# Kernel tuning notes

Hardware: AMD Instinct MI355X
Metric: run time of the kernel (lower is better)

Reference implementation:

```python
import jax, jax.numpy as jnp
import numpy as np

B, TV, TE = 128, 32, 64
VOCAB, EMB, H, REPR, NET, MAXLEN = 1024, 256, 512, 128, 8, 32


def setup_inputs() -> dict:
    key = jax.random.key(0)
    ks = jax.random.split(key, 26)
    g = lambda i, shape: jax.random.normal(ks[i], shape, dtype=jnp.float32) * 0.05
    return dict(
        input_vertex=jax.random.randint(ks[0], (B, TV), 0, VOCAB),
        input_edge=jax.random.randint(ks[1], (B, TE, 3), 0, NET),
        vertex_emb=g(2, (VOCAB, EMB)),
        v_Wi=g(3, (3 * H, EMB)), v_Wh=g(4, (3 * H, H)), v_bi=g(5, (3 * H,)), v_bh=g(6, (3 * H,)),
        vout_W=g(7, (VOCAB, H)), vout_b=g(8, (VOCAB,)),
        vrep_W=g(9, (REPR, H)), vrep_b=g(10, (REPR,)),
        edge_emb=g(11, (MAXLEN, EMB)),
        e_Wi=g(12, (3 * H, 2 * EMB)), e_Wh=g(13, (3 * H, H)), e_bi=g(14, (3 * H,)), e_bh=g(15, (3 * H,)),
        erep_W=g(16, (REPR, H)), erep_b=g(17, (REPR,)),
        etype_W=g(18, (NET, REPR)), etype_b=g(19, (NET,)),
        src_w=g(20, (REPR,)), src_b=g(21, ()),
        dst_w=g(22, (REPR,)), dst_b=g(23, ()),
    )


def _gru_scan(X, Wi, Wh, bi, bh):
    # X: [T, B, D] -> hidden states [T, B, H]; torch GRUCell gate order r,z,n
    gi = jnp.einsum('tbd,gd->tbg', X, Wi) + bi  # precompute input projections
    h0 = jnp.zeros((X.shape[1], Wh.shape[1]), X.dtype)

    def step(h, gi_t):
        gh = h @ Wh.T + bh
        ir, iz, inn = jnp.split(gi_t, 3, axis=-1)
        hr, hz, hn = jnp.split(gh, 3, axis=-1)
        r = jax.nn.sigmoid(ir + hr)
        z = jax.nn.sigmoid(iz + hz)
        n = jnp.tanh(inn + r * hn)
        h_new = (1.0 - z) * n + z * h
        return h_new, h_new

    _, hs = jax.lax.scan(step, h0, gi)
    return hs


def reference(input_vertex, input_edge, vertex_emb, v_Wi, v_Wh, v_bi, v_bh,
              vout_W, vout_b, vrep_W, vrep_b, edge_emb, e_Wi, e_Wh, e_bi, e_bh,
              erep_W, erep_b, etype_W, etype_b, src_w, src_b, dst_w, dst_b):
    # ---- vertex RNN ----
    Ve = vertex_emb[input_vertex].transpose(1, 0, 2)          # [Tv, B, emb]
    hv = _gru_scan(Ve, v_Wi, v_Wh, v_bi, v_bh)                # [Tv, B, H]
    O_vertex = jnp.einsum('tbh,vh->bvt', hv, vout_W) + vout_b[None, :, None]  # [B, vocab, Tv]
    vrep = jnp.einsum('tbh,rh->tbr', hv, vrep_W) + vrep_b     # [Tv, B, repr]

    # ---- edge RNN ----
    E = jnp.concatenate([edge_emb[input_edge[:, :, 0]],
                         edge_emb[input_edge[:, :, 1]]], axis=2)  # [B, Te, 2*emb]
    he = _gru_scan(E.transpose(1, 0, 2), e_Wi, e_Wh, e_bi, e_bh)  # [Te, B, H]
    e = jnp.einsum('tbh,rh->tbr', he, erep_W) + erep_b            # [Te, B, repr]
    O_edge_type = jnp.einsum('ebr,kr->bke', e, etype_W) + etype_b[None, :, None]  # [B, n_et, Te]

    # ---- edge-vertex additive attention: tanh(e + v) ----
    u = jnp.tanh(e[:, None] + vrep[None])                     # [Te, Tv, B, repr]
    osrc = jnp.einsum('evbr,r->bve', u, src_w) + src_b        # [B, Tv, Te]
    odst = jnp.einsum('evbr,r->bve', u, dst_w) + dst_b        # [B, Tv, Te]
    O_edge = jnp.stack([osrc, odst], axis=2)                  # [B, Tv, 2, Te]

    return O_vertex, O_edge, O_edge_type
```

## Files before the change

kernel.cpp:

```cpp
#include <hip/hip_runtime.h>
#include <hip/hip_bf16.h>


typedef __bf16 bf16_t;
typedef bf16_t bf16x8 __attribute__((ext_vector_type(8)));
typedef bf16_t bf16x4 __attribute__((ext_vector_type(4)));
typedef float  f32x4  __attribute__((ext_vector_type(4)));

#define OFF_GIV  0ull
#define OFF_GIE  6291456ull
#define OFF_HV   18874368ull
#define OFF_HE   20971520ull
#define OFF_VREP 25165824ull
#define OFF_EREP 25690112ull
#define OFF_HBUF 26738688ull
#define FLAG_BYTE_OFF 54001664ull
#define GICNT_BYTE_OFF 54001920ull
#define OFF_CVT  27002880ull
#define CVT_VEMB  0ull
#define CVT_EEMB  262144ull
#define CVT_VWI   270336ull
#define CVT_EWI   663552ull
#define CVT_VWH   1449984ull
#define CVT_EWH   2236416ull
#define CVT_VOUT  3022848ull
#define CVT_VREPW 3547136ull
#define CVT_EREPW 3612672ull

#define OUT_OV 0ull
#define OUT_OE 4194304ull
#define OUT_OT 4718592ull

__device__ __forceinline__ float fsigmoid(float x) {
    float e = __builtin_amdgcn_exp2f(-x * 1.4426950408889634f);
    return __builtin_amdgcn_rcpf(1.0f + e);
}
__device__ __forceinline__ float ftanh(float x) {
    x = fminf(x, 15.0f);
    float e = __builtin_amdgcn_exp2f(x * 2.8853900817779268f);
    return (e - 1.0f) * __builtin_amdgcn_rcpf(e + 1.0f);
}

__global__ __launch_bounds__(256) void prep_kernel(
    const float* __restrict__ vemb, const float* __restrict__ eemb,
    const float* __restrict__ vwi,  const float* __restrict__ ewi,
    const float* __restrict__ vwh,  const float* __restrict__ ewh,
    const float* __restrict__ voutw, const float* __restrict__ vrepw,
    const float* __restrict__ erepw, bf16_t* __restrict__ cvt,
    int* __restrict__ gicnt)
{
    int blk = blockIdx.x;
    if (blk >= 3592) {
        if (threadIdx.x < 128) gicnt[threadIdx.x] = 0;
        return;
    }
    const float* src; bf16_t* dst; int lb;
    if (blk < 256)       { src = vemb;  dst = cvt + CVT_VEMB;  lb = blk; }
    else if (blk < 264)  { src = eemb;  dst = cvt + CVT_EEMB;  lb = blk - 256; }
    else if (blk < 648)  { src = vwi;   dst = cvt + CVT_VWI;   lb = blk - 264; }
    else if (blk < 1416) { src = ewi;   dst = cvt + CVT_EWI;   lb = blk - 648; }
    else if (blk < 2184) { src = vwh;   dst = cvt + CVT_VWH;   lb = blk - 1416; }
    else if (blk < 2952) { src = ewh;   dst = cvt + CVT_EWH;   lb = blk - 2184; }
    else if (blk < 3464) { src = voutw; dst = cvt + CVT_VOUT;  lb = blk - 2952; }
    else if (blk < 3528) { src = vrepw; dst = cvt + CVT_VREPW; lb = blk - 3464; }
    else                 { src = erepw; dst = cvt + CVT_EREPW; lb = blk - 3528; }
    int idx = lb * 1024 + threadIdx.x * 4;
    float4 v = *(const float4*)(src + idx);
    bf16x4 o;
    o[0] = (bf16_t)v.x; o[1] = (bf16_t)v.y; o[2] = (bf16_t)v.z; o[3] = (bf16_t)v.w;
    *(bf16x4*)(dst + idx) = o;
}

template<int GATHER, int K>
__device__ __forceinline__ void produce_gi(
    const bf16_t* __restrict__ W, const float* __restrict__ bias,
    bf16_t* __restrict__ C, const int* __restrict__ gidx,
    const bf16_t* __restrict__ emb, int* __restrict__ cnt, int bx, int nbase)
{
    constexpr int K32 = K / 32;
    const int tid = threadIdx.x, lane = tid & 63, wv = tid >> 6;
    const int r16 = lane & 15, quad = lane >> 4, koff = quad * 8;
    const int mbase = bx * 512 + wv * 64;

    const bf16_t* ap0[4];
    const bf16_t* ap1[4];
#pragma unroll
    for (int i = 0; i < 4; ++i) {
        int row = mbase + i * 16 + r16;
        int b = row & 127, t = row >> 7;
        if (GATHER == 1) {
            ap0[i] = emb + (size_t)gidx[b * 32 + t] * 256 + koff;
            ap1[i] = ap0[i];
        } else {
            int c = (b * 64 + t) * 3;
            ap0[i] = emb + (size_t)gidx[c] * 256 + koff;
            ap1[i] = emb + (size_t)gidx[c + 1] * 256 + koff;
        }
    }
    const bf16_t* bp[4];
#pragma unroll
    for (int j = 0; j < 4; ++j)
        bp[j] = W + (size_t)(nbase + j * 16 + r16) * K + koff;

    f32x4 acc[4][4];
#pragma unroll
    for (int i = 0; i < 4; ++i)
#pragma unroll
        for (int j = 0; j < 4; ++j) acc[i][j] = (f32x4){0.f, 0.f, 0.f, 0.f};

    for (int kc = 0; kc < K32; ++kc) {
        bf16x8 a[4], b[4];
#pragma unroll
        for (int i = 0; i < 4; ++i) {
            const bf16_t* p;
            if (GATHER == 2) p = (kc < 8) ? (ap0[i] + kc * 32) : (ap1[i] + (kc - 8) * 32);
            else             p = ap0[i] + kc * 32;
            a[i] = *(const bf16x8*)p;
        }
#pragma unroll
        for (int j = 0; j < 4; ++j) b[j] = *(const bf16x8*)(bp[j] + kc * 32);
#pragma unroll
        for (int i = 0; i < 4; ++i)
#pragma unroll
            for (int j = 0; j < 4; ++j)
                acc[i][j] = __builtin_amdgcn_mfma_f32_16x16x32_bf16(a[i], b[j], acc[i][j], 0, 0, 0);
    }

#pragma unroll
    for (int j = 0; j < 4; ++j) {
        int col = nbase + j * 16 + r16;
        float bf = bias[col];
#pragma unroll
        for (int i = 0; i < 4; ++i) {
#pragma unroll
            for (int q = 0; q < 4; ++q) {
                int row = mbase + i * 16 + quad * 4 + q;
                bf16_t hb = (bf16_t)(acc[i][j][q] + bf);
                __hip_atomic_store((unsigned short*)(C + (size_t)row * 1536 + col),
                                   __builtin_bit_cast(unsigned short, hb),
                                   __ATOMIC_RELAXED, __HIP_MEMORY_SCOPE_AGENT);
            }
        }
    }
    __builtin_amdgcn_s_waitcnt(0);
    __syncthreads();
    if (tid < 4)
        __hip_atomic_fetch_add(&cnt[bx * 4 + tid], 1,
                               __ATOMIC_RELAXED, __HIP_MEMORY_SCOPE_AGENT);
}

template<int OUTMODE, int K>
__device__ __forceinline__ void consume_gemm(
    const bf16_t* __restrict__ A, const bf16_t* __restrict__ W,
    const float* __restrict__ bias, void* __restrict__ Cv,
    int N, int bx, int nbase)
{
    constexpr int K32 = K / 32;
    const int tid = threadIdx.x, lane = tid & 63, wv = tid >> 6;
    const int r16 = lane & 15, quad = lane >> 4, koff = quad * 8;
    const int mbase = bx * 512 + wv * 64;

    const bf16_t* ap[4];
#pragma unroll
    for (int i = 0; i < 4; ++i)
        ap[i] = A + (size_t)(mbase + i * 16 + r16) * K + koff;
    const bf16_t* bp[4];
#pragma unroll
    for (int j = 0; j < 4; ++j)
        bp[j] = W + (size_t)(nbase + j * 16 + r16) * K + koff;

    f32x4 acc[4][4];
#pragma unroll
    for (int i = 0; i < 4; ++i)
#pragma unroll
        for (int j = 0; j < 4; ++j) acc[i][j] = (f32x4){0.f, 0.f, 0.f, 0.f};

    for (int kc = 0; kc < K32; ++kc) {
        bf16x8 a[4], b[4];
#pragma unroll
        for (int i = 0; i < 4; ++i) a[i] = *(const bf16x8*)(ap[i] + kc * 32);
#pragma unroll
        for (int j = 0; j < 4; ++j) b[j] = *(const bf16x8*)(bp[j] + kc * 32);
#pragma unroll
        for (int i = 0; i < 4; ++i)
#pragma unroll
            for (int j = 0; j < 4; ++j)
                acc[i][j] = __builtin_amdgcn_mfma_f32_16x16x32_bf16(a[i], b[j], acc[i][j], 0, 0, 0);
    }

#pragma unroll
    for (int j = 0; j < 4; ++j) {
        int col = nbase + j * 16 + r16;
        float bf = bias[col];
#pragma unroll
        for (int i = 0; i < 4; ++i) {
            int rowq = mbase + i * 16 + quad * 4;
            if (OUTMODE == 1) {
                int b = rowq >> 5, t0 = rowq & 31;
                float4 v4;
                v4.x = acc[i][j][0] + bf; v4.y = acc[i][j][1] + bf;
                v4.z = acc[i][j][2] + bf; v4.w = acc[i][j][3] + bf;
                *(float4*)((float*)Cv + ((size_t)(b * 1024) + col) * 32 + t0) = v4;
            } else {
                bf16_t* C = (bf16_t*)Cv;
#pragma unroll
                for (int q = 0; q < 4; ++q)
                    C[(size_t)(rowq + q) * N + col] = (bf16_t)(acc[i][j][q] + bf);
            }
        }
    }
}

__device__ __forceinline__ void gate_on(int* p, int thresh) {
    if (threadIdx.x == 0) {
        while (__hip_atomic_load(p, __ATOMIC_RELAXED,
                                 __HIP_MEMORY_SCOPE_AGENT) < thresh)
            __builtin_amdgcn_s_sleep(8);
    }
    __syncthreads();
    asm volatile("" ::: "memory");
}

__global__ __launch_bounds__(512) void fused_scan(
    bf16_t* __restrict__ giV, bf16_t* __restrict__ giE,
    const bf16_t* __restrict__ WhV, const bf16_t* __restrict__ WhE,
    const float* __restrict__ bhV, const float* __restrict__ bhE,
    bf16_t* __restrict__ hV, bf16_t* __restrict__ hE,
    bf16_t* __restrict__ hbuf, int* __restrict__ flags, int* __restrict__ gicnt,
    const int* __restrict__ ivtx, const int* __restrict__ iedg,
    const bf16_t* __restrict__ vemb, const bf16_t* __restrict__ eemb,
    const bf16_t* __restrict__ vwi, const bf16_t* __restrict__ ewi,
    const float* __restrict__ vbi, const float* __restrict__ ebi,
    const bf16_t* __restrict__ voutw, const float* __restrict__ voutb,
    const bf16_t* __restrict__ vrepw, const float* __restrict__ vrepb,
    const bf16_t* __restrict__ erepw, const float* __restrict__ erepb,
    bf16_t* __restrict__ vrep, bf16_t* __restrict__ erep,
    float* __restrict__ out)
{
    __shared__ __align__(16) bf16_t hbf[2][16][520];
    __shared__ char ldspad[31744];
    const int bid = blockIdx.x;
    if ((int)gridDim.x < 0) ldspad[threadIdx.x] = 0;

    if (bid >= 64) {
        if (bid < 256) {
            int g2 = bid - 64;
            produce_gi<1, 256>(vwi, vbi, giV, ivtx, vemb, gicnt, g2 & 7, (g2 >> 3) * 64);
        } else if (bid < 640) {
            int g3 = bid - 256;
            produce_gi<2, 512>(ewi, ebi, giE, iedg, eemb, gicnt + 32, g3 & 15, (g3 >> 4) * 64);
        } else if (bid < 784) {
            gate_on(&gicnt[96], 32);
            if (bid < 768) {
                int cb = bid - 640;
                consume_gemm<1, 512>(hV, voutw, voutb, out, 1024, cb & 7, (cb >> 3) * 64);
            } else {
                int cb = bid - 768;
                consume_gemm<0, 512>(hV, vrepw, vrepb, vrep, 128, cb & 7, (cb >> 3) * 64);
            }
        } else {
            gate_on(&gicnt[97], 32);
            int cb = bid - 784;
            consume_gemm<0, 512>(hE, erepw, erepb, erep, 128, cb & 15, (cb >> 4) * 64);
        }
        return;
    }

    const int role = bid >> 5;
    const int lb   = bid & 31;
    const int g    = lb & 7;
    const int s    = lb >> 3;
    const bf16_t* gi = role ? giE : giV;
    const bf16_t* Wh = role ? WhE : WhV;
    const float*  bh = role ? bhE : bhV;
    bf16_t* hout = role ? hE : hV;
    const int T = role ? 64 : 32;
    const int slot = role * 8 + g;
    bf16_t* buf0 = hbuf + (size_t)slot * 2 * 8192;
    int* fl = flags + slot * 4;
    int* gc = role ? (gicnt + 32) : gicnt;
    int* done = role ? &gicnt[97] : &gicnt[96];
    const int bb = g * 16;

    const int tid = threadIdx.x, lane = tid & 63, wv = tid >> 6;
    const int r16 = lane & 15, quad = lane >> 4, koff = quad * 8;
    const int j = s * 128 + wv * 16 + r16;
    const int rs0 = (s + 1) & 3, rs1 = (s + 2) & 3, rs2 = (s + 3) & 3;

    bf16x8 wfrag[3][16];
#pragma unroll
    for (int gate = 0; gate < 3; ++gate) {
        const bf16_t* wrow = Wh + ((size_t)(gate * 512 + j)) * 512 + koff;
#pragma unroll
        for (int kc = 0; kc < 16; ++kc)
            wfrag[gate][kc] = *(const bf16x8*)(wrow + kc * 32);
    }
    const float bhr = bh[j], bhz = bh[512 + j], bhn = bh[1024 + j];
    float hq[4] = {0.f, 0.f, 0.f, 0.f};

    for (int i = tid; i < 16 * 512; i += 512)
        hbf[0][i >> 9][i & 511] = (bf16_t)0.f;

    const int arow = tid >> 5, au = tid & 31;

    for (int t = 0; t < T; ++t) {
        if (wv == 0) {
            while (__hip_atomic_load(&gc[t], __ATOMIC_RELAXED,
                                     __HIP_MEMORY_SCOPE_AGENT) < 24)
                __builtin_amdgcn_s_sleep(2);
        }
        __syncthreads();
        asm volatile("" ::: "memory");

        float gv[3][4];
#pragma unroll
        for (int gg = 0; gg < 3; ++gg)
#pragma unroll
            for (int q = 0; q < 4; ++q)
                gv[gg][q] = (float)gi[((size_t)(t * 128 + bb + quad * 4 + q)) * 1536
                                      + gg * 512 + j];

        if (t > 0) {
            if (wv == 1) {
                while (!__all((int)(__hip_atomic_load(&fl[lane & 3], __ATOMIC_RELAXED,
                                                      __HIP_MEMORY_SCOPE_AGENT) >= t))) { }
            }
            __syncthreads();
            asm volatile("" ::: "memory");
            unsigned long long* src = (unsigned long long*)(buf0 + (size_t)(t & 1) * 8192);
            unsigned long long vv[3];
            vv[0] = __hip_atomic_load(src + arow * 128 + rs0 * 32 + au, __ATOMIC_RELAXED, __HIP_MEMORY_SCOPE_AGENT);
            vv[1] = __hip_atomic_load(src + arow * 128 + rs1 * 32 + au, __ATOMIC_RELAXED, __HIP_MEMORY_SCOPE_AGENT);
            vv[2] = __hip_atomic_load(src + arow * 128 + rs2 * 32 + au, __ATOMIC_RELAXED, __HIP_MEMORY_SCOPE_AGENT);
            *(unsigned long long*)&hbf[t & 1][arow][rs0 * 128 + au * 4] = vv[0];
            *(unsigned long long*)&hbf[t & 1][arow][rs1 * 128 + au * 4] = vv[1];
            *(unsigned long long*)&hbf[t & 1][arow][rs2 * 128 + au * 4] = vv[2];
        }
        __syncthreads();

        const bf16_t (*cur)[520] = hbf[t & 1];
        f32x4 ar = {0.f,0.f,0.f,0.f}, az = {0.f,0.f,0.f,0.f}, an = {0.f,0.f,0.f,0.f};
#pragma unroll
        for (int kc = 0; kc < 16; ++kc) {
            bf16x8 a = *(const bf16x8*)&cur[r16][kc * 32 + koff];
            ar = __builtin_amdgcn_mfma_f32_16x16x32_bf16(a, wfrag[0][kc], ar, 0, 0, 0);
            az = __builtin_amdgcn_mfma_f32_16x16x32_bf16(a, wfrag[1][kc], az, 0, 0, 0);
            an = __builtin_amdgcn_mfma_f32_16x16x32_bf16(a, wfrag[2][kc], an, 0, 0, 0);
        }

        bf16_t hb4[4];
#pragma unroll
        for (int q = 0; q < 4; ++q) {
            float r = fsigmoid(gv[0][q] + ar[q] + bhr);
            float z = fsigmoid(gv[1][q] + az[q] + bhz);
            float n = ftanh(gv[2][q] + r * (an[q] + bhn));
            float hnew = (1.0f - z) * n + z * hq[q];
            hq[q] = hnew;
            hb4[q] = (bf16_t)hnew;
        }

        bf16_t (*nxt)[520] = hbf[(t + 1) & 1];
#pragma unroll
        for (int q = 0; q < 4; ++q) nxt[quad * 4 + q][j] = hb4[q];

        if (t + 1 < T) {
            bf16_t* dstg = buf0 + (size_t)((t + 1) & 1) * 8192;
#pragma unroll
            for (int q = 0; q < 4; ++q)
                __hip_atomic_store((unsigned short*)(dstg + (quad * 4 + q) * 512 + j),
                                   __builtin_bit_cast(unsigned short, hb4[q]),
                                   __ATOMIC_RELAXED, __HIP_MEMORY_SCOPE_AGENT);
            __builtin_amdgcn_s_waitcnt(0);
            __syncthreads();
            if (tid == 0)
                __hip_atomic_store(&fl[s], t + 1,
                                   __ATOMIC_RELAXED, __HIP_MEMORY_SCOPE_AGENT);
        } else {
            __syncthreads();
        }
#pragma unroll
        for (int q = 0; q < 4; ++q)
            __hip_atomic_store(
                (unsigned short*)(hout + ((size_t)((bb + quad * 4 + q) * T + t)) * 512 + j),
                __builtin_bit_cast(unsigned short, hb4[q]),
                __ATOMIC_RELAXED, __HIP_MEMORY_SCOPE_AGENT);
    }

    __builtin_amdgcn_s_waitcnt(0);
    __syncthreads();
    if (tid == 0)
        __hip_atomic_fetch_add(done, 1, __ATOMIC_RELAXED, __HIP_MEMORY_SCOPE_AGENT);
}

__global__ __launch_bounds__(256) void etype_kernel(
    const bf16_t* __restrict__ erep, const float* __restrict__ W,
    const float* __restrict__ bias, float* __restrict__ out)
{
    int o = blockIdx.x * 256 + threadIdx.x;
    int te = o & 63, k = (o >> 6) & 7, b = o >> 9;
    float sacc = bias[k];
    const bf16_t* e = erep + ((size_t)(b * 64 + te)) * 128;
    const float* w = W + k * 128;
#pragma unroll 8
    for (int r = 0; r < 128; ++r) sacc += (float)e[r] * w[r];
    out[OUT_OT + o] = sacc;
}

__global__ __launch_bounds__(256) void attn_kernel(
    const bf16_t* __restrict__ erep, const bf16_t* __restrict__ vrep,
    const float* __restrict__ src_w, const float* __restrict__ src_b,
    const float* __restrict__ dst_w, const float* __restrict__ dst_b,
    float* __restrict__ out)
{
    int b = blockIdx.x >> 1, half = blockIdx.x & 1;
    __shared__ float es[32][129], vs[32][129], swf[128], dwf[128];
    int tid = threadIdx.x;
    for (int f = tid; f < 32 * 128; f += 256) {
        int i = f >> 7, r = f & 127;
        es[i][r] = (float)erep[((size_t)(b * 64 + half * 32 + i)) * 128 + r];
        vs[i][r] = (float)vrep[((size_t)(b * 32 + i)) * 128 + r];
    }
    if (tid < 128) { swf[tid] = src_w[tid]; dwf[tid] = dst_w[tid]; }
    __syncthreads();
    float sb = src_b[0], db = dst_b[0];
    for (int p = tid; p < 1024; p += 256) {
        int te = p & 31, tv = p >> 5;
        float sacc = 0.f, dacc = 0.f;
#pragma unroll 4
        for (int r = 0; r < 128; ++r) {
            float u = ftanh(es[te][r] + vs[tv][r]);
            sacc += u * swf[r];
            dacc += u * dwf[r];
        }
        int teg = half * 32 + te;
        size_t base = OUT_OE + ((size_t)(b * 32 + tv) * 2) * 64;
        out[base + teg]      = sacc + sb;
        out[base + 64 + teg] = dacc + db;
    }
}

extern "C" void kernel_launch(void* const* d_in, const int* in_sizes, int n_in,
                              void* d_out, int out_size, void* d_ws, size_t ws_size,
                              hipStream_t stream)
{
    const int*   input_vertex = (const int*)d_in[0];
    const int*   input_edge   = (const int*)d_in[1];
    const float* vertex_emb   = (const float*)d_in[2];
    const float* v_Wi  = (const float*)d_in[3];
    const float* v_Wh  = (const float*)d_in[4];
    const float* v_bi  = (const float*)d_in[5];
    const float* v_bh  = (const float*)d_in[6];
    const float* vout_W = (const float*)d_in[7];
    const float* vout_b = (const float*)d_in[8];
    const float* vrep_W = (const float*)d_in[9];
    const float* vrep_b = (const float*)d_in[10];
    const float* edge_emb = (const float*)d_in[11];
    const float* e_Wi  = (const float*)d_in[12];
    const float* e_Wh  = (const float*)d_in[13];
    const float* e_bi  = (const float*)d_in[14];
    const float* e_bh  = (const float*)d_in[15];
    const float* erep_W = (const float*)d_in[16];
    const float* erep_b = (const float*)d_in[17];
    const float* etype_W = (const float*)d_in[18];
    const float* etype_b = (const float*)d_in[19];
    const float* src_w = (const float*)d_in[20];
    const float* src_b = (const float*)d_in[21];
    const float* dst_w = (const float*)d_in[22];
    const float* dst_b = (const float*)d_in[23];

    bf16_t* ws   = (bf16_t*)d_ws;
    bf16_t* giV  = ws + OFF_GIV;
    bf16_t* giE  = ws + OFF_GIE;
    bf16_t* hV   = ws + OFF_HV;
    bf16_t* hE   = ws + OFF_HE;
    bf16_t* vrep = ws + OFF_VREP;
    bf16_t* erep = ws + OFF_EREP;
    bf16_t* hbuf = ws + OFF_HBUF;
    bf16_t* cvt  = ws + OFF_CVT;
    int*    flags = (int*)((char*)d_ws + FLAG_BYTE_OFF);
    int*    gicnt = (int*)((char*)d_ws + GICNT_BYTE_OFF);
    float*  out  = (float*)d_out;

    prep_kernel<<<3593, 256, 0, stream>>>(vertex_emb, edge_emb, v_Wi, e_Wi, v_Wh, e_Wh,
                                          vout_W, vrep_W, erep_W, cvt, gicnt);

    fused_scan<<<816, 512, 0, stream>>>(
        giV, giE, cvt + CVT_VWH, cvt + CVT_EWH, v_bh, e_bh, hV, hE,
        hbuf, flags, gicnt, input_vertex, input_edge,
        cvt + CVT_VEMB, cvt + CVT_EEMB, cvt + CVT_VWI, cvt + CVT_EWI,
        v_bi, e_bi,
        cvt + CVT_VOUT, vout_b, cvt + CVT_VREPW, vrep_b,
        cvt + CVT_EREPW, erep_b, vrep, erep, out);

    etype_kernel<<<256, 256, 0, stream>>>(erep, etype_W, etype_b, out);
    attn_kernel<<<256, 256, 0, stream>>>(erep, vrep, src_w, src_b, dst_w, dst_b, out);
}
```

Before: 447.7 us.

## Split fused persistent scan into separate produce, GRU scan and consume kernels

Replaces the single persistent fused kernel, which overlapped input-projection GEMMs, the recurrent scans and the output GEMMs through atomic counters, with three separate launches. The GRU scan now spreads each batch group over 8 blocks instead of 4, and each block splits the K dimension between two wave halves that are reduced through shared memory. This halves the per-wave recurrent weight registers and gives more parallelism per step, at the cost of an extra LDS reduction and barrier each step, more cross-block flag polling, and losing the overlap between the producer GEMM and the scan.

```diff
diff --git a/kernel.cpp b/kernel.cpp
--- a/kernel.cpp
+++ b/kernel.cpp
@@ -15,7 +15,6 @@
 #define OFF_EREP 25690112ull
 #define OFF_HBUF 26738688ull
 #define FLAG_BYTE_OFF 54001664ull
-#define GICNT_BYTE_OFF 54001920ull
 #define OFF_CVT  27002880ull
 #define CVT_VEMB  0ull
 #define CVT_EEMB  262144ull
@@ -46,14 +45,9 @@
     const float* __restrict__ vwi,  const float* __restrict__ ewi,
     const float* __restrict__ vwh,  const float* __restrict__ ewh,
     const float* __restrict__ voutw, const float* __restrict__ vrepw,
-    const float* __restrict__ erepw, bf16_t* __restrict__ cvt,
-    int* __restrict__ gicnt)
+    const float* __restrict__ erepw, bf16_t* __restrict__ cvt)
 {
     int blk = blockIdx.x;
-    if (blk >= 3592) {
-        if (threadIdx.x < 128) gicnt[threadIdx.x] = 0;
-        return;
-    }
     const float* src; bf16_t* dst; int lb;
     if (blk < 256)       { src = vemb;  dst = cvt + CVT_VEMB;  lb = blk; }
     else if (blk < 264)  { src = eemb;  dst = cvt + CVT_EEMB;  lb = blk - 256; }
@@ -75,7 +69,7 @@
 __device__ __forceinline__ void produce_gi(
     const bf16_t* __restrict__ W, const float* __restrict__ bias,
     bf16_t* __restrict__ C, const int* __restrict__ gidx,
-    const bf16_t* __restrict__ emb, int* __restrict__ cnt, int bx, int nbase)
+    const bf16_t* __restrict__ emb, int bx, int nbase)
 {
     constexpr int K32 = K / 32;
     const int tid = threadIdx.x, lane = tid & 63, wv = tid >> 6;
@@ -135,18 +129,160 @@
 #pragma unroll
             for (int q = 0; q < 4; ++q) {
                 int row = mbase + i * 16 + quad * 4 + q;
-                bf16_t hb = (bf16_t)(acc[i][j][q] + bf);
-                __hip_atomic_store((unsigned short*)(C + (size_t)row * 1536 + col),
-                                   __builtin_bit_cast(unsigned short, hb),
+                C[(size_t)row * 1536 + col] = (bf16_t)(acc[i][j][q] + bf);
+            }
+        }
+    }
+}
+
+__global__ __launch_bounds__(512) void produce_kernel(
+    bf16_t* __restrict__ giV, bf16_t* __restrict__ giE,
+    const int* __restrict__ ivtx, const int* __restrict__ iedg,
+    const bf16_t* __restrict__ vemb, const bf16_t* __restrict__ eemb,
+    const bf16_t* __restrict__ vwi, const bf16_t* __restrict__ ewi,
+    const float* __restrict__ vbi, const float* __restrict__ ebi)
+{
+    int bid = blockIdx.x;
+    if (bid < 192) {
+        produce_gi<1, 256>(vwi, vbi, giV, ivtx, vemb, bid & 7, (bid >> 3) * 64);
+    } else {
+        int g3 = bid - 192;
+        produce_gi<2, 512>(ewi, ebi, giE, iedg, eemb, g3 & 15, (g3 >> 4) * 64);
+    }
+}
+
+__global__ __launch_bounds__(512)
+__attribute__((amdgpu_waves_per_eu(2, 2)))
+void gru_scan(
+    const bf16_t* __restrict__ giV, const bf16_t* __restrict__ giE,
+    const bf16_t* __restrict__ WhV, const bf16_t* __restrict__ WhE,
+    const float* __restrict__ bhV, const float* __restrict__ bhE,
+    bf16_t* __restrict__ hV, bf16_t* __restrict__ hE,
+    bf16_t* __restrict__ hbuf, int* __restrict__ flags)
+{
+    __shared__ __align__(16) bf16_t hbf[2][16][520];
+    __shared__ __align__(16) f32x4 red[4][3][64];
+    const int bid = blockIdx.x;
+
+    const int role = bid >> 6;
+    const int lb   = bid & 63;
+    const int g    = lb & 7;
+    const int s    = lb >> 3;
+    const bf16_t* gi = role ? giE : giV;
+    const bf16_t* Wh = role ? WhE : WhV;
+    const float*  bh = role ? bhE : bhV;
+    bf16_t* hout = role ? hE : hV;
+    const int T = role ? 64 : 32;
+    const int slot = role * 8 + g;
+    bf16_t* buf0 = hbuf + (size_t)slot * 2 * 8192;
+    int* fl = flags + slot * 8;
+    const int bb = g * 16;
+
+    const int tid = threadIdx.x, lane = tid & 63, wv = tid >> 6;
+    const int team = wv >> 1, half = wv & 1;
+    const int r16 = lane & 15, quad = lane >> 4, koff = quad * 8;
+    const int j = s * 64 + team * 16 + r16;
+    const int kbase = half * 256;
+
+    bf16x8 wfrag[3][8];
+#pragma unroll
+    for (int gate = 0; gate < 3; ++gate) {
+        const bf16_t* wrow = Wh + ((size_t)(gate * 512 + j)) * 512 + kbase + koff;
+#pragma unroll
+        for (int kc = 0; kc < 8; ++kc)
+            wfrag[gate][kc] = *(const bf16x8*)(wrow + kc * 32);
+    }
+    const float bhr = bh[j], bhz = bh[512 + j], bhn = bh[1024 + j];
+    float hq[4] = {0.f, 0.f, 0.f, 0.f};
+
+    for (int i = tid; i < 16 * 512; i += 512)
+        hbf[0][i >> 9][i & 511] = (bf16_t)0.f;
+
+    for (int t = 0; t < T; ++t) {
+        if (t > 0) {
+            if (wv == 1) {
+                while (!__all((int)(__hip_atomic_load(&fl[lane & 7], __ATOMIC_RELAXED,
+                                                      __HIP_MEMORY_SCOPE_AGENT) >= t))) { }
+            }
+            __syncthreads();
+            asm volatile("" ::: "memory");
+            unsigned long long* src = (unsigned long long*)(buf0 + (size_t)(t & 1) * 8192);
+#pragma unroll
+            for (int k = 0; k < 4; ++k) {
+                int u = tid + k * 512;
+                unsigned long long vv = __hip_atomic_load(src + u, __ATOMIC_RELAXED,
+                                                          __HIP_MEMORY_SCOPE_AGENT);
+                *(unsigned long long*)&hbf[t & 1][u >> 7][(u & 127) * 4] = vv;
+            }
+        }
+        __syncthreads();
+
+        float gv[3][4];
+        if (half == 0) {
+#pragma unroll
+            for (int gg = 0; gg < 3; ++gg)
+#pragma unroll
+                for (int q = 0; q < 4; ++q)
+                    gv[gg][q] = (float)gi[((size_t)(t * 128 + bb + quad * 4 + q)) * 1536
+                                          + gg * 512 + j];
+        }
+
+        const bf16_t (*cur)[520] = hbf[t & 1];
+        f32x4 ar = {0.f,0.f,0.f,0.f}, az = {0.f,0.f,0.f,0.f}, an = {0.f,0.f,0.f,0.f};
+#pragma unroll
+        for (int kc = 0; kc < 8; ++kc) {
+            bf16x8 a = *(const bf16x8*)&cur[r16][kbase + kc * 32 + koff];
+            ar = __builtin_amdgcn_mfma_f32_16x16x32_bf16(a, wfrag[0][kc], ar, 0, 0, 0);
+            az = __builtin_amdgcn_mfma_f32_16x16x32_bf16(a, wfrag[1][kc], az, 0, 0, 0);
+            an = __builtin_amdgcn_mfma_f32_16x16x32_bf16(a, wfrag[2][kc], an, 0, 0, 0);
+        }
+
+        if (half == 1) {
+            red[team][0][lane] = ar;
+            red[team][1][lane] = az;
+            red[team][2][lane] = an;
+        }
+        __syncthreads();
+
+        bf16_t hb4[4];
+        if (half == 0) {
+            ar += red[team][0][lane];
+            az += red[team][1][lane];
+            an += red[team][2][lane];
+#pragma unroll
+            for (int q = 0; q < 4; ++q) {
+                float r = fsigmoid(gv[0][q] + ar[q] + bhr);
+                float z = fsigmoid(gv[1][q] + az[q] + bhz);
+                float n = ftanh(gv[2][q] + r * (an[q] + bhn));
+                float hnew = (1.0f - z) * n + z * hq[q];
+                hq[q] = hnew;
+                hb4[q] = (bf16_t)hnew;
+            }
+            if (t + 1 < T) {
+                bf16_t* dstg = buf0 + (size_t)((t + 1) & 1) * 8192;
+#pragma unroll
+                for (int q = 0; q < 4; ++q)
+                    __hip_atomic_store((unsigned short*)(dstg + (quad * 4 + q) * 512 + j),
+                                       __builtin_bit_cast(unsigned short, hb4[q]),
+                                       __ATOMIC_RELAXED, __HIP_MEMORY_SCOPE_AGENT);
+            }
+        }
+
+        if (t + 1 < T) {
+            __builtin_amdgcn_s_waitcnt(0);
+            __syncthreads();
+            if (tid == 0)
+                __hip_atomic_store(&fl[s], t + 1,
                                    __ATOMIC_RELAXED, __HIP_MEMORY_SCOPE_AGENT);
-            }
-        }
-    }
-    __builtin_amdgcn_s_waitcnt(0);
-    __syncthreads();
-    if (tid < 4)
-        __hip_atomic_fetch_add(&cnt[bx * 4 + tid], 1,
-                               __ATOMIC_RELAXED, __HIP_MEMORY_SCOPE_AGENT);
+        } else {
+            __syncthreads();
+        }
+        if (half == 0) {
+#pragma unroll
+            for (int q = 0; q < 4; ++q)
+                hout[((size_t)((bb + quad * 4 + q) * T + t)) * 512 + j] = hb4[q];
+        }
+    }
 }
 
 template<int OUTMODE, int K>
@@ -211,185 +347,24 @@
     }
 }
 
-__device__ __forceinline__ void gate_on(int* p, int thresh) {
-    if (threadIdx.x == 0) {
-        while (__hip_atomic_load(p, __ATOMIC_RELAXED,
-                                 __HIP_MEMORY_SCOPE_AGENT) < thresh)
-            __builtin_amdgcn_s_sleep(8);
-    }
-    __syncthreads();
-    asm volatile("" ::: "memory");
-}
-
-__global__ __launch_bounds__(512) void fused_scan(
-    bf16_t* __restrict__ giV, bf16_t* __restrict__ giE,
-    const bf16_t* __restrict__ WhV, const bf16_t* __restrict__ WhE,
-    const float* __restrict__ bhV, const float* __restrict__ bhE,
-    bf16_t* __restrict__ hV, bf16_t* __restrict__ hE,
-    bf16_t* __restrict__ hbuf, int* __restrict__ flags, int* __restrict__ gicnt,
-    const int* __restrict__ ivtx, const int* __restrict__ iedg,
-    const bf16_t* __restrict__ vemb, const bf16_t* __restrict__ eemb,
-    const bf16_t* __restrict__ vwi, const bf16_t* __restrict__ ewi,
-    const float* __restrict__ vbi, const float* __restrict__ ebi,
+__global__ __launch_bounds__(512) void consume_kernel(
+    const bf16_t* __restrict__ hV, const bf16_t* __restrict__ hE,
     const bf16_t* __restrict__ voutw, const float* __restrict__ voutb,
     const bf16_t* __restrict__ vrepw, const float* __restrict__ vrepb,
     const bf16_t* __restrict__ erepw, const float* __restrict__ erepb,
     bf16_t* __restrict__ vrep, bf16_t* __restrict__ erep,
     float* __restrict__ out)
 {
-    __shared__ __align__(16) bf16_t hbf[2][16][520];
-    __shared__ char ldspad[31744];
-    const int bid = blockIdx.x;
-    if ((int)gridDim.x < 0) ldspad[threadIdx.x] = 0;
-
-    if (bid >= 64) {
-        if (bid < 256) {
-            int g2 = bid - 64;
-            produce_gi<1, 256>(vwi, vbi, giV, ivtx, vemb, gicnt, g2 & 7, (g2 >> 3) * 64);
-        } else if (bid < 640) {
-            int g3 = bid - 256;
-            produce_gi<2, 512>(ewi, ebi, giE, iedg, eemb, gicnt + 32, g3 & 15, (g3 >> 4) * 64);
-        } else if (bid < 784) {
-            gate_on(&gicnt[96], 32);
-            if (bid < 768) {
-                int cb = bid - 640;
-                consume_gemm<1, 512>(hV, voutw, voutb, out, 1024, cb & 7, (cb >> 3) * 64);
-            } else {
-                int cb = bid - 768;
-                consume_gemm<0, 512>(hV, vrepw, vrepb, vrep, 128, cb & 7, (cb >> 3) * 64);
-            }
-        } else {
-            gate_on(&gicnt[97], 32);
-            int cb = bid - 784;
-            consume_gemm<0, 512>(hE, erepw, erepb, erep, 128, cb & 15, (cb >> 4) * 64);
-        }
-        return;
-    }
-
-    const int role = bid >> 5;
-    const int lb   = bid & 31;
-    const int g    = lb & 7;
-    const int s    = lb >> 3;
-    const bf16_t* gi = role ? giE : giV;
-    const bf16_t* Wh = role ? WhE : WhV;
-    const float*  bh = role ? bhE : bhV;
-    bf16_t* hout = role ? hE : hV;
-    const int T = role ? 64 : 32;
-    const int slot = role * 8 + g;
-    bf16_t* buf0 = hbuf + (size_t)slot * 2 * 8192;
-    int* fl = flags + slot * 4;
-    int* gc = role ? (gicnt + 32) : gicnt;
-    int* done = role ? &gicnt[97] : &gicnt[96];
-    const int bb = g * 16;
-
-    const int tid = threadIdx.x, lane = tid & 63, wv = tid >> 6;
-    const int r16 = lane & 15, quad = lane >> 4, koff = quad * 8;
-    const int j = s * 128 + wv * 16 + r16;
-    const int rs0 = (s + 1) & 3, rs1 = (s + 2) & 3, rs2 = (s + 3) & 3;
-
-    bf16x8 wfrag[3][16];
-#pragma unroll
-    for (int gate = 0; gate < 3; ++gate) {
-        const bf16_t* wrow = Wh + ((size_t)(gate * 512 + j)) * 512 + koff;
-#pragma unroll
-        for (int kc = 0; kc < 16; ++kc)
-            wfrag[gate][kc] = *(const bf16x8*)(wrow + kc * 32);
-    }
-    const float bhr = bh[j], bhz = bh[512 + j], bhn = bh[1024 + j];
-    float hq[4] = {0.f, 0.f, 0.f, 0.f};
-
-    for (int i = tid; i < 16 * 512; i += 512)
-        hbf[0][i >> 9][i & 511] = (bf16_t)0.f;
-
-    const int arow = tid >> 5, au = tid & 31;
-
-    for (int t = 0; t < T; ++t) {
-        if (wv == 0) {
-            while (__hip_atomic_load(&gc[t], __ATOMIC_RELAXED,
-                                     __HIP_MEMORY_SCOPE_AGENT) < 24)
-                __builtin_amdgcn_s_sleep(2);
-        }
-        __syncthreads();
-        asm volatile("" ::: "memory");
-
-        float gv[3][4];
-#pragma unroll
-        for (int gg = 0; gg < 3; ++gg)
-#pragma unroll
-            for (int q = 0; q < 4; ++q)
-                gv[gg][q] = (float)gi[((size_t)(t * 128 + bb + quad * 4 + q)) * 1536
-                                      + gg * 512 + j];
-
-        if (t > 0) {
-            if (wv == 1) {
-                while (!__all((int)(__hip_atomic_load(&fl[lane & 3], __ATOMIC_RELAXED,
-                                                      __HIP_MEMORY_SCOPE_AGENT) >= t))) { }
-            }
-            __syncthreads();
-            asm volatile("" ::: "memory");
-            unsigned long long* src = (unsigned long long*)(buf0 + (size_t)(t & 1) * 8192);
-            unsigned long long vv[3];
-            vv[0] = __hip_atomic_load(src + arow * 128 + rs0 * 32 + au, __ATOMIC_RELAXED, __HIP_MEMORY_SCOPE_AGENT);
-            vv[1] = __hip_atomic_load(src + arow * 128 + rs1 * 32 + au, __ATOMIC_RELAXED, __HIP_MEMORY_SCOPE_AGENT);
-            vv[2] = __hip_atomic_load(src + arow * 128 + rs2 * 32 + au, __ATOMIC_RELAXED, __HIP_MEMORY_SCOPE_AGENT);
-            *(unsigned long long*)&hbf[t & 1][arow][rs0 * 128 + au * 4] = vv[0];
-            *(unsigned long long*)&hbf[t & 1][arow][rs1 * 128 + au * 4] = vv[1];
-            *(unsigned long long*)&hbf[t & 1][arow][rs2 * 128 + au * 4] = vv[2];
-        }
-        __syncthreads();
-
-        const bf16_t (*cur)[520] = hbf[t & 1];
-        f32x4 ar = {0.f,0.f,0.f,0.f}, az = {0.f,0.f,0.f,0.f}, an = {0.f,0.f,0.f,0.f};
-#pragma unroll
-        for (int kc = 0; kc < 16; ++kc) {
-            bf16x8 a = *(const bf16x8*)&cur[r16][kc * 32 + koff];
-            ar = __builtin_amdgcn_mfma_f32_16x16x32_bf16(a, wfrag[0][kc], ar, 0, 0, 0);
-            az = __builtin_amdgcn_mfma_f32_16x16x32_bf16(a, wfrag[1][kc], az, 0, 0, 0);
-            an = __builtin_amdgcn_mfma_f32_16x16x32_bf16(a, wfrag[2][kc], an, 0, 0, 0);
-        }
-
-        bf16_t hb4[4];
-#pragma unroll
-        for (int q = 0; q < 4; ++q) {
-            float r = fsigmoid(gv[0][q] + ar[q] + bhr);
-            float z = fsigmoid(gv[1][q] + az[q] + bhz);
-            float n = ftanh(gv[2][q] + r * (an[q] + bhn));
-            float hnew = (1.0f - z) * n + z * hq[q];
-            hq[q] = hnew;
-            hb4[q] = (bf16_t)hnew;
-        }
-
-        bf16_t (*nxt)[520] = hbf[(t + 1) & 1];
-#pragma unroll
-        for (int q = 0; q < 4; ++q) nxt[quad * 4 + q][j] = hb4[q];
-
-        if (t + 1 < T) {
-            bf16_t* dstg = buf0 + (size_t)((t + 1) & 1) * 8192;
-#pragma unroll
-            for (int q = 0; q < 4; ++q)
-                __hip_atomic_store((unsigned short*)(dstg + (quad * 4 + q) * 512 + j),
-                                   __builtin_bit_cast(unsigned short, hb4[q]),
-                                   __ATOMIC_RELAXED, __HIP_MEMORY_SCOPE_AGENT);
-            __builtin_amdgcn_s_waitcnt(0);
-            __syncthreads();
-            if (tid == 0)
-                __hip_atomic_store(&fl[s], t + 1,
-                                   __ATOMIC_RELAXED, __HIP_MEMORY_SCOPE_AGENT);
-        } else {
-            __syncthreads();
-        }
-#pragma unroll
-        for (int q = 0; q < 4; ++q)
-            __hip_atomic_store(
-                (unsigned short*)(hout + ((size_t)((bb + quad * 4 + q) * T + t)) * 512 + j),
-                __builtin_bit_cast(unsigned short, hb4[q]),
-                __ATOMIC_RELAXED, __HIP_MEMORY_SCOPE_AGENT);
-    }
-
-    __builtin_amdgcn_s_waitcnt(0);
-    __syncthreads();
-    if (tid == 0)
-        __hip_atomic_fetch_add(done, 1, __ATOMIC_RELAXED, __HIP_MEMORY_SCOPE_AGENT);
+    int bid = blockIdx.x;
+    if (bid < 128) {
+        consume_gemm<1, 512>(hV, voutw, voutb, out, 1024, bid & 7, (bid >> 3) * 64);
+    } else if (bid < 144) {
+        int cb = bid - 128;
+        consume_gemm<0, 512>(hV, vrepw, vrepb, vrep, 128, cb & 7, (cb >> 3) * 64);
+    } else {
+        int cb = bid - 144;
+        consume_gemm<0, 512>(hE, erepw, erepb, erep, 128, cb & 15, (cb >> 4) * 64);
+    }
 }
 
 __global__ __launch_bounds__(256) void etype_kernel(
@@ -478,19 +453,21 @@
     bf16_t* hbuf = ws + OFF_HBUF;
     bf16_t* cvt  = ws + OFF_CVT;
     int*    flags = (int*)((char*)d_ws + FLAG_BYTE_OFF);
-    int*    gicnt = (int*)((char*)d_ws + GICNT_BYTE_OFF);
     float*  out  = (float*)d_out;
 
-    prep_kernel<<<3593, 256, 0, stream>>>(vertex_emb, edge_emb, v_Wi, e_Wi, v_Wh, e_Wh,
-                                          vout_W, vrep_W, erep_W, cvt, gicnt);
-
-    fused_scan<<<816, 512, 0, stream>>>(
-        giV, giE, cvt + CVT_VWH, cvt + CVT_EWH, v_bh, e_bh, hV, hE,
-        hbuf, flags, gicnt, input_vertex, input_edge,
-        cvt + CVT_VEMB, cvt + CVT_EEMB, cvt + CVT_VWI, cvt + CVT_EWI,
-        v_bi, e_bi,
-        cvt + CVT_VOUT, vout_b, cvt + CVT_VREPW, vrep_b,
-        cvt + CVT_EREPW, erep_b, vrep, erep, out);
+    prep_kernel<<<3592, 256, 0, stream>>>(vertex_emb, edge_emb, v_Wi, e_Wi, v_Wh, e_Wh,
+                                          vout_W, vrep_W, erep_W, cvt);
+
+    produce_kernel<<<576, 512, 0, stream>>>(giV, giE, input_vertex, input_edge,
+                                            cvt + CVT_VEMB, cvt + CVT_EEMB,
+                                            cvt + CVT_VWI, cvt + CVT_EWI, v_bi, e_bi);
+
+    gru_scan<<<128, 512, 0, stream>>>(giV, giE, cvt + CVT_VWH, cvt + CVT_EWH,
+                                      v_bh, e_bh, hV, hE, hbuf, flags);
+
+    consume_kernel<<<176, 512, 0, stream>>>(hV, hE, cvt + CVT_VOUT, vout_b,
+                                            cvt + CVT_VREPW, vrep_b,
+                                            cvt + CVT_EREPW, erep_b, vrep, erep, out);
 
     etype_kernel<<<256, 256, 0, stream>>>(erep, etype_W, etype_b, out);
     attn_kernel<<<256, 256, 0, stream>>>(erep, vrep, src_w, src_b, dst_w, dst_b, out);
```

Measured after the change: 480.5 us. +7.3%, slower.

## Split GRU recurrence across twice the blocks with split-K wave-pair reduction

Applied to the files above, without the earlier changes.

Each batch group's recurrent matmul is now spread over 8 column slices instead of 4, so 128 scan blocks each own 64 hidden columns. Within a block, pairs of waves split the K dimension in half and reduce their partial results through LDS, which halves each wave's register-resident weights and MFMA chain per step. The h exchange now reads the whole 16x512 state from global each step, and the producer blocks are remapped to a different tiling. The cost is more cross-block flag polling per step (8 slices), an extra LDS reduction barrier, and more global traffic per step.

```diff
diff --git a/kernel.cpp b/kernel.cpp
--- a/kernel.cpp
+++ b/kernel.cpp
@@ -6,6 +6,7 @@
 typedef bf16_t bf16x8 __attribute__((ext_vector_type(8)));
 typedef bf16_t bf16x4 __attribute__((ext_vector_type(4)));
 typedef float  f32x4  __attribute__((ext_vector_type(4)));
+typedef unsigned long long ull_t;
 
 #define OFF_GIV  0ull
 #define OFF_GIE  6291456ull
@@ -14,8 +15,8 @@
 #define OFF_VREP 25165824ull
 #define OFF_EREP 25690112ull
 #define OFF_HBUF 26738688ull
-#define FLAG_BYTE_OFF 54001664ull
-#define GICNT_BYTE_OFF 54001920ull
+#define FLAG_BYTE_OFF  54001664ull
+#define GICNT_BYTE_OFF 54002176ull
 #define OFF_CVT  27002880ull
 #define CVT_VEMB  0ull
 #define CVT_EEMB  262144ull
@@ -237,37 +238,40 @@
     bf16_t* __restrict__ vrep, bf16_t* __restrict__ erep,
     float* __restrict__ out)
 {
-    __shared__ __align__(16) bf16_t hbf[2][16][520];
-    __shared__ char ldspad[31744];
+    __shared__ __align__(16) bf16_t hbf[32][520];
+    __shared__ __align__(16) f32x4 red[4][3][64];
+    __shared__ char ldspad[38400];
     const int bid = blockIdx.x;
     if ((int)gridDim.x < 0) ldspad[threadIdx.x] = 0;
 
-    if (bid >= 64) {
-        if (bid < 256) {
-            int g2 = bid - 64;
-            produce_gi<1, 256>(vwi, vbi, giV, ivtx, vemb, gicnt, g2 & 7, (g2 >> 3) * 64);
-        } else if (bid < 640) {
-            int g3 = bid - 256;
-            produce_gi<2, 512>(ewi, ebi, giE, iedg, eemb, gicnt + 32, g3 & 15, (g3 >> 4) * 64);
-        } else if (bid < 784) {
-            gate_on(&gicnt[96], 32);
-            if (bid < 768) {
-                int cb = bid - 640;
+    if (bid >= 128) {
+        if (bid < 512) {
+            int g3 = bid - 128;
+            int bx = g3 / 24, nb = g3 - bx * 24;
+            produce_gi<2, 512>(ewi, ebi, giE, iedg, eemb, gicnt + 32, bx, nb * 64);
+        } else if (bid < 704) {
+            int g2 = bid - 512;
+            int bx = g2 / 24, nb = g2 - bx * 24;
+            produce_gi<1, 256>(vwi, vbi, giV, ivtx, vemb, gicnt, bx, nb * 64);
+        } else if (bid < 848) {
+            gate_on(&gicnt[96], 64);
+            if (bid < 832) {
+                int cb = bid - 704;
                 consume_gemm<1, 512>(hV, voutw, voutb, out, 1024, cb & 7, (cb >> 3) * 64);
             } else {
-                int cb = bid - 768;
+                int cb = bid - 832;
                 consume_gemm<0, 512>(hV, vrepw, vrepb, vrep, 128, cb & 7, (cb >> 3) * 64);
             }
         } else {
-            gate_on(&gicnt[97], 32);
-            int cb = bid - 784;
+            gate_on(&gicnt[97], 64);
+            int cb = bid - 848;
             consume_gemm<0, 512>(hE, erepw, erepb, erep, 128, cb & 15, (cb >> 4) * 64);
         }
         return;
     }
 
-    const int role = bid >> 5;
-    const int lb   = bid & 31;
+    const int role = bid >> 6;
+    const int lb   = bid & 63;
     const int g    = lb & 7;
     const int s    = lb >> 3;
     const bf16_t* gi = role ? giE : giV;
@@ -276,35 +280,35 @@
     bf16_t* hout = role ? hE : hV;
     const int T = role ? 64 : 32;
     const int slot = role * 8 + g;
-    bf16_t* buf0 = hbuf + (size_t)slot * 2 * 8192;
-    int* fl = flags + slot * 4;
+    bf16_t* buf0 = hbuf + (size_t)slot * 16384;
+    int* fl = flags + slot * 8;
     int* gc = role ? (gicnt + 32) : gicnt;
     int* done = role ? &gicnt[97] : &gicnt[96];
     const int bb = g * 16;
 
-    const int tid = threadIdx.x, lane = tid & 63, wv = tid >> 6;
+    const int tid = threadIdx.x, lane = tid & 63, w = tid >> 6;
+    const int team = w >> 1, half = w & 1;
     const int r16 = lane & 15, quad = lane >> 4, koff = quad * 8;
-    const int j = s * 128 + wv * 16 + r16;
-    const int rs0 = (s + 1) & 3, rs1 = (s + 2) & 3, rs2 = (s + 3) & 3;
-
-    bf16x8 wfrag[3][16];
+    const int j = s * 64 + team * 16 + r16;
+    const int kbase = half * 256;
+
+    bf16x8 wfrag[3][8];
 #pragma unroll
     for (int gate = 0; gate < 3; ++gate) {
-        const bf16_t* wrow = Wh + ((size_t)(gate * 512 + j)) * 512 + koff;
-#pragma unroll
-        for (int kc = 0; kc < 16; ++kc)
+        const bf16_t* wrow = Wh + ((size_t)(gate * 512 + j)) * 512 + kbase + koff;
+#pragma unroll
+        for (int kc = 0; kc < 8; ++kc)
             wfrag[gate][kc] = *(const bf16x8*)(wrow + kc * 32);
     }
     const float bhr = bh[j], bhz = bh[512 + j], bhn = bh[1024 + j];
     float hq[4] = {0.f, 0.f, 0.f, 0.f};
 
-    for (int i = tid; i < 16 * 512; i += 512)
-        hbf[0][i >> 9][i & 511] = (bf16_t)0.f;
-
-    const int arow = tid >> 5, au = tid & 31;
+    for (int u = tid; u < 16 * 520; u += 512)
+        ((bf16_t*)hbf)[u] = (bf16_t)0.f;
+    __syncthreads();
 
     for (int t = 0; t < T; ++t) {
-        if (wv == 0) {
+        if (w == 0) {
             while (__hip_atomic_load(&gc[t], __ATOMIC_RELAXED,
                                      __HIP_MEMORY_SCOPE_AGENT) < 24)
                 __builtin_amdgcn_s_sleep(2);
@@ -313,63 +317,75 @@
         asm volatile("" ::: "memory");
 
         float gv[3][4];
-#pragma unroll
-        for (int gg = 0; gg < 3; ++gg)
-#pragma unroll
-            for (int q = 0; q < 4; ++q)
-                gv[gg][q] = (float)gi[((size_t)(t * 128 + bb + quad * 4 + q)) * 1536
-                                      + gg * 512 + j];
+        if (half == 0) {
+#pragma unroll
+            for (int gg = 0; gg < 3; ++gg)
+#pragma unroll
+                for (int q = 0; q < 4; ++q)
+                    gv[gg][q] = (float)gi[((size_t)(t * 128 + bb + quad * 4 + q)) * 1536
+                                          + gg * 512 + j];
+        }
 
         if (t > 0) {
-            if (wv == 1) {
-                while (!__all((int)(__hip_atomic_load(&fl[lane & 3], __ATOMIC_RELAXED,
+            if (w == 1) {
+                while (!__all((int)(__hip_atomic_load(&fl[lane & 7], __ATOMIC_RELAXED,
                                                       __HIP_MEMORY_SCOPE_AGENT) >= t))) { }
             }
             __syncthreads();
             asm volatile("" ::: "memory");
-            unsigned long long* src = (unsigned long long*)(buf0 + (size_t)(t & 1) * 8192);
-            unsigned long long vv[3];
-            vv[0] = __hip_atomic_load(src + arow * 128 + rs0 * 32 + au, __ATOMIC_RELAXED, __HIP_MEMORY_SCOPE_AGENT);
-            vv[1] = __hip_atomic_load(src + arow * 128 + rs1 * 32 + au, __ATOMIC_RELAXED, __HIP_MEMORY_SCOPE_AGENT);
-            vv[2] = __hip_atomic_load(src + arow * 128 + rs2 * 32 + au, __ATOMIC_RELAXED, __HIP_MEMORY_SCOPE_AGENT);
-            *(unsigned long long*)&hbf[t & 1][arow][rs0 * 128 + au * 4] = vv[0];
-            *(unsigned long long*)&hbf[t & 1][arow][rs1 * 128 + au * 4] = vv[1];
-            *(unsigned long long*)&hbf[t & 1][arow][rs2 * 128 + au * 4] = vv[2];
+            ull_t* src = (ull_t*)(buf0 + (size_t)(t & 1) * 8192);
+#pragma unroll
+            for (int k = 0; k < 4; ++k) {
+                int u = tid + k * 512;
+                ull_t vv = __hip_atomic_load(src + u, __ATOMIC_RELAXED,
+                                             __HIP_MEMORY_SCOPE_AGENT);
+                *(ull_t*)&hbf[u >> 7][(u & 127) * 4] = vv;
+            }
         }
         __syncthreads();
 
-        const bf16_t (*cur)[520] = hbf[t & 1];
         f32x4 ar = {0.f,0.f,0.f,0.f}, az = {0.f,0.f,0.f,0.f}, an = {0.f,0.f,0.f,0.f};
 #pragma unroll
-        for (int kc = 0; kc < 16; ++kc) {
-            bf16x8 a = *(const bf16x8*)&cur[r16][kc * 32 + koff];
+        for (int kc = 0; kc < 8; ++kc) {
+            bf16x8 a = *(const bf16x8*)&hbf[r16][kbase + kc * 32 + koff];
             ar = __builtin_amdgcn_mfma_f32_16x16x32_bf16(a, wfrag[0][kc], ar, 0, 0, 0);
             az = __builtin_amdgcn_mfma_f32_16x16x32_bf16(a, wfrag[1][kc], az, 0, 0, 0);
             an = __builtin_amdgcn_mfma_f32_16x16x32_bf16(a, wfrag[2][kc], an, 0, 0, 0);
         }
 
+        if (half == 1) {
+            red[team][0][lane] = ar;
+            red[team][1][lane] = az;
+            red[team][2][lane] = an;
+        }
+        __syncthreads();
+
         bf16_t hb4[4];
-#pragma unroll
-        for (int q = 0; q < 4; ++q) {
-            float r = fsigmoid(gv[0][q] + ar[q] + bhr);
-            float z = fsigmoid(gv[1][q] + az[q] + bhz);
-            float n = ftanh(gv[2][q] + r * (an[q] + bhn));
-            float hnew = (1.0f - z) * n + z * hq[q];
-            hq[q] = hnew;
-            hb4[q] = (bf16_t)hnew;
-        }
-
-        bf16_t (*nxt)[520] = hbf[(t + 1) & 1];
-#pragma unroll
-        for (int q = 0; q < 4; ++q) nxt[quad * 4 + q][j] = hb4[q];
+        if (half == 0) {
+            ar += red[team][0][lane];
+            az += red[team][1][lane];
+            an += red[team][2][lane];
+#pragma unroll
+            for (int q = 0; q < 4; ++q) {
+                float r = fsigmoid(gv[0][q] + ar[q] + bhr);
+                float z = fsigmoid(gv[1][q] + az[q] + bhz);
+                float n = ftanh(gv[2][q] + r * (an[q] + bhn));
+                float hnew = (1.0f - z) * n + z * hq[q];
+                hq[q] = hnew;
+                hb4[q] = (bf16_t)hnew;
+            }
+            if (t + 1 < T) {
+                bf16_t* dstg = buf0 + (size_t)((t + 1) & 1) * 8192;
+#pragma unroll
+                for (int q = 0; q < 4; ++q)
+                    __hip_atomic_store(
+                        (unsigned short*)(dstg + (quad * 4 + q) * 512 + j),
+                        __builtin_bit_cast(unsigned short, hb4[q]),
+                        __ATOMIC_RELAXED, __HIP_MEMORY_SCOPE_AGENT);
+            }
+        }
 
         if (t + 1 < T) {
-            bf16_t* dstg = buf0 + (size_t)((t + 1) & 1) * 8192;
-#pragma unroll
-            for (int q = 0; q < 4; ++q)
-                __hip_atomic_store((unsigned short*)(dstg + (quad * 4 + q) * 512 + j),
-                                   __builtin_bit_cast(unsigned short, hb4[q]),
-                                   __ATOMIC_RELAXED, __HIP_MEMORY_SCOPE_AGENT);
             __builtin_amdgcn_s_waitcnt(0);
             __syncthreads();
             if (tid == 0)
@@ -378,12 +394,14 @@
         } else {
             __syncthreads();
         }
-#pragma unroll
-        for (int q = 0; q < 4; ++q)
-            __hip_atomic_store(
-                (unsigned short*)(hout + ((size_t)((bb + quad * 4 + q) * T + t)) * 512 + j),
-                __builtin_bit_cast(unsigned short, hb4[q]),
-                __ATOMIC_RELAXED, __HIP_MEMORY_SCOPE_AGENT);
+        if (half == 0) {
+#pragma unroll
+            for (int q = 0; q < 4; ++q)
+                __hip_atomic_store(
+                    (unsigned short*)(hout + ((size_t)((bb + quad * 4 + q) * T + t)) * 512 + j),
+                    __builtin_bit_cast(unsigned short, hb4[q]),
+                    __ATOMIC_RELAXED, __HIP_MEMORY_SCOPE_AGENT);
+        }
     }
 
     __builtin_amdgcn_s_waitcnt(0);
@@ -484,7 +502,7 @@
     prep_kernel<<<3593, 256, 0, stream>>>(vertex_emb, edge_emb, v_Wi, e_Wi, v_Wh, e_Wh,
                                           vout_W, vrep_W, erep_W, cvt, gicnt);
 
-    fused_scan<<<816, 512, 0, stream>>>(
+    fused_scan<<<880, 512, 0, stream>>>(
         giV, giE, cvt + CVT_VWH, cvt + CVT_EWH, v_bh, e_bh, hV, hE,
         hbuf, flags, gicnt, input_vertex, input_edge,
         cvt + CVT_VEMB, cvt + CVT_EEMB, cvt + CVT_VWI, cvt + CVT_EWI,
```

New measurement: 428.1 us. 1.05x faster.
